# Optimization experiments

Measured on AMD Instinct MI355X. Metric: run time of the kernel, lower is better.

## Reference

```python
import jax, jax.numpy as jnp
import numpy as np
from jax import lax

N_NODES = 50000
N_EDGES = 800000
FEAT = 16
HID = 64
K = 32
N_CLASSES = 8


def _dconv(Xc, W, b, src, dst, norm_out, norm_in):
    """Dual-direction diffusion (Chebyshev-style) graph convolution.
    Xc: [N, Fin], W: [2, K, Fin, HID], norm_*: per-edge weights."""
    N = Xc.shape[0]

    def prop(x, s, d, ne):
        # out[i] = sum_{e: d[e]=i} ne[e] * x[s[e]]
        return jax.ops.segment_sum(x[s] * ne[:, None], d, num_segments=N)

    # k = 0 term (identity support, both directions)
    H = Xc @ (W[0, 0] + W[1, 0])
    # k = 1 term
    T1o = prop(Xc, src, dst, norm_out)   # forward diffusion
    T1i = prop(Xc, dst, src, norm_in)    # reverse diffusion
    H = H + T1o @ W[0, 1] + T1i @ W[1, 1]

    def step(carry, Wk):
        T0o, T1o, T0i, T1i, Hacc = carry
        T2o = 2.0 * prop(T1o, src, dst, norm_out) - T0o
        T2i = 2.0 * prop(T1i, dst, src, norm_in) - T0i
        Hacc = Hacc + T2o @ Wk[0] + T2i @ Wk[1]
        return (T1o, T2o, T1i, T2i, Hacc), None

    Wtail = jnp.stack([W[0, 2:], W[1, 2:]], axis=1)  # [K-2, 2, Fin, HID]
    (_, _, _, _, H), _ = lax.scan(step, (Xc, T1o, Xc, T1i, H), Wtail)
    return H + b


def setup_inputs() -> dict:
    key = jax.random.key(0)
    ks = jax.random.split(key, 8)
    Fin = FEAT + HID
    wscale = 1.0 / np.sqrt(Fin * K)
    x = jax.random.normal(ks[0], (N_NODES, FEAT), jnp.float32)
    edge_index = jax.random.randint(ks[1], (2, N_EDGES), 0, N_NODES, jnp.int64)
    W_z = jax.random.normal(ks[2], (2, K, Fin, HID), jnp.float32) * wscale
    W_r = jax.random.normal(ks[3], (2, K, Fin, HID), jnp.float32) * wscale
    W_h = jax.random.normal(ks[4], (2, K, Fin, HID), jnp.float32) * wscale
    lin_w = jax.random.normal(ks[5], (HID, N_CLASSES), jnp.float32) / np.sqrt(HID)
    return {
        "x": x, "edge_index": edge_index,
        "W_z": W_z, "b_z": jnp.zeros((HID,), jnp.float32),
        "W_r": W_r, "b_r": jnp.zeros((HID,), jnp.float32),
        "W_h": W_h, "b_h": jnp.zeros((HID,), jnp.float32),
        "lin_w": lin_w, "lin_b": jnp.zeros((N_CLASSES,), jnp.float32),
    }


def reference(x, edge_index, W_z, b_z, W_r, b_r, W_h, b_h, lin_w, lin_b):
    N = x.shape[0]
    src, dst = edge_index[0], edge_index[1]
    w = jnp.ones(src.shape[0], x.dtype)
    deg_out = jax.ops.segment_sum(w, src, num_segments=N)
    deg_in = jax.ops.segment_sum(w, dst, num_segments=N)
    inv = lambda d: jnp.where(d > 0, 1.0 / d, 0.0)
    norm_out = inv(deg_out)[src]  # per-edge 1/out-deg(source), forward walk
    norm_in = inv(deg_in)[dst]    # per-edge 1/in-deg(target), reverse walk

    # DCRNN GRU cell, single step, H initialized to zeros
    H0 = jnp.zeros((N, HID), x.dtype)
    Xc = jnp.concatenate([x, H0], axis=1)
    Z = jax.nn.sigmoid(_dconv(Xc, W_z, b_z, src, dst, norm_out, norm_in))
    R = jax.nn.sigmoid(_dconv(Xc, W_r, b_r, src, dst, norm_out, norm_in))
    Xh = jnp.concatenate([x, H0 * R], axis=1)
    Ht = jnp.tanh(_dconv(Xh, W_h, b_h, src, dst, norm_out, norm_in))
    H = Z * H0 + (1.0 - Z) * Ht

    return jax.nn.relu(H) @ lin_w + lin_b
```

## Files before the change

### kernel.cpp

```cpp
#include <hip/hip_runtime.h>
#include <math.h>

#define N_NODES 50000
#define N_EDGES 800000
#define FEAT    16
#define HID     64
#define KORD    32
#define NCLS    8

#define WSL     5120
#define SLOT    (N_NODES * FEAT)

typedef __attribute__((ext_vector_type(8))) short bf8_t;
typedef __attribute__((ext_vector_type(4))) float f32x4;

static constexpr size_t Aln(size_t x) { return (x + 255) & ~size_t(255); }

static constexpr size_t OFF_DEG_OUT = 0;
static constexpr size_t OFF_DEG_IN  = OFF_DEG_OUT + Aln(N_NODES * 4);
static constexpr size_t OFF_CUR_DST = OFF_DEG_IN  + Aln(N_NODES * 4);
static constexpr size_t OFF_CUR_SRC = OFF_CUR_DST + Aln(N_NODES * 4);
static constexpr size_t ZERO_BYTES  = OFF_CUR_SRC + Aln(N_NODES * 4);
static constexpr size_t OFF_OFF_DST = ZERO_BYTES;
static constexpr size_t OFF_OFF_SRC = OFF_OFF_DST + Aln((N_NODES + 1) * 4);
static constexpr size_t OFF_CSRD    = OFF_OFF_SRC + Aln((N_NODES + 1) * 4);
static constexpr size_t OFF_CSRS    = OFF_CSRD + Aln(N_EDGES * 4);
static constexpr size_t OFF_SLAB    = OFF_CSRS + Aln(N_EDGES * 4);
static constexpr size_t OFF_BSZH    = OFF_SLAB + Aln((size_t)64 * SLOT * 4);
static constexpr size_t OFF_BSZL    = OFF_BSZH + Aln((size_t)32 * 8 * 64 * 8 * 2);
static constexpr size_t WS_TOTAL    = OFF_BSZL + Aln((size_t)32 * 8 * 64 * 8 * 2);

__device__ __forceinline__ ushort f2bf(float v) {
    unsigned int b = __float_as_uint(v);
    b += 0x7FFFu + ((b >> 16) & 1u);
    return (ushort)(b >> 16);
}
__device__ __forceinline__ float bf2f(ushort h) {
    return __uint_as_float((unsigned int)h << 16);
}

__global__ void count_deg_kernel(const int* __restrict__ ei,
                                 int* __restrict__ deg_out, int* __restrict__ deg_in) {
    int e4 = blockIdx.x * blockDim.x + threadIdx.x;
    if (e4 * 4 >= N_EDGES) return;
    int4 s = *(const int4*)&ei[e4 * 4];
    int4 d = *(const int4*)&ei[N_EDGES + e4 * 4];
    atomicAdd(&deg_out[s.x], 1); atomicAdd(&deg_out[s.y], 1);
    atomicAdd(&deg_out[s.z], 1); atomicAdd(&deg_out[s.w], 1);
    atomicAdd(&deg_in[d.x], 1);  atomicAdd(&deg_in[d.y], 1);
    atomicAdd(&deg_in[d.z], 1);  atomicAdd(&deg_in[d.w], 1);
}

__global__ __launch_bounds__(1024) void scan_kernel(const int* __restrict__ degA, int* __restrict__ offA,
                                                    const int* __restrict__ degB, int* __restrict__ offB) {
    const int* deg = blockIdx.x ? degB : degA;
    int* off = blockIdx.x ? offB : offA;
    __shared__ int wsum[16];
    __shared__ int s_run;
    const int t = threadIdx.x, lane = t & 63, wid = t >> 6;
    if (t == 0) s_run = 0;
    __syncthreads();
    for (int base = 0; base < N_NODES; base += 1024) {
        int i = base + t;
        int v = (i < N_NODES) ? deg[i] : 0;
        int xv = v;
        #pragma unroll
        for (int d = 1; d < 64; d <<= 1) {
            int tt = __shfl_up(xv, d, 64);
            if (lane >= d) xv += tt;
        }
        if (lane == 63) wsum[wid] = xv;
        __syncthreads();
        int add = s_run;
        for (int w = 0; w < wid; ++w) add += wsum[w];
        if (i < N_NODES) off[i] = add + xv - v;
        __syncthreads();
        if (t == 1023) s_run = add + xv;
        __syncthreads();
    }
    if (t == 0) off[N_NODES] = s_run;
}

__global__ void fill_csr_kernel(const int* __restrict__ ei,
                                const int* __restrict__ deg_out, const int* __restrict__ deg_in,
                                const int* __restrict__ off_dst, const int* __restrict__ off_src,
                                int* __restrict__ cur_dst, int* __restrict__ cur_src,
                                unsigned int* __restrict__ csrd, unsigned int* __restrict__ csrs) {
    int e = blockIdx.x * blockDim.x + threadIdx.x;
    if (e >= N_EDGES) return;
    int s = ei[e], d = ei[N_EDGES + e];
    int p = off_dst[d] + atomicAdd(&cur_dst[d], 1);
    csrd[p] = ((unsigned int)deg_out[s] << 16) | (unsigned int)s;
    int q = off_src[s] + atomicAdd(&cur_src[s], 1);
    csrs[q] = ((unsigned int)deg_in[d] << 16) | (unsigned int)d;
}

__device__ __forceinline__ float4 gather4d(const unsigned int* __restrict__ csr, int beg, int end,
                                           int u, int fq, const float* __restrict__ src) {
    float4 acc = {0.f, 0.f, 0.f, 0.f};
    for (int e0 = beg; e0 < end; e0 += 16) {
        int ea = e0 + u, eb = e0 + 4 + u, ec = e0 + 8 + u, ed = e0 + 12 + u;
        unsigned int pa = (ea < end) ? csr[ea] : 0x10000u;
        unsigned int pb = (eb < end) ? csr[eb] : 0x10000u;
        unsigned int pc = (ec < end) ? csr[ec] : 0x10000u;
        unsigned int pd = (ed < end) ? csr[ed] : 0x10000u;
        float wa = (ea < end) ? 1.0f / (float)(pa >> 16) : 0.0f;
        float wb = (eb < end) ? 1.0f / (float)(pb >> 16) : 0.0f;
        float wc = (ec < end) ? 1.0f / (float)(pc >> 16) : 0.0f;
        float wd = (ed < end) ? 1.0f / (float)(pd >> 16) : 0.0f;
        const float4 ra = *(const float4*)&src[(pa & 0xFFFFu) * FEAT + fq * 4];
        const float4 rb = *(const float4*)&src[(pb & 0xFFFFu) * FEAT + fq * 4];
        const float4 rc = *(const float4*)&src[(pc & 0xFFFFu) * FEAT + fq * 4];
        const float4 rd = *(const float4*)&src[(pd & 0xFFFFu) * FEAT + fq * 4];
        acc.x += wa * ra.x + wb * rb.x + wc * rc.x + wd * rd.x;
        acc.y += wa * ra.y + wb * rb.y + wc * rc.y + wd * rd.y;
        acc.z += wa * ra.z + wb * rb.z + wc * rc.z + wd * rd.z;
        acc.w += wa * ra.w + wb * rb.w + wc * rc.w + wd * rd.w;
    }
    return acc;
}

__device__ __forceinline__ float4 reduce_u(float4 a) {
    a.x += __shfl_xor(a.x, 4); a.y += __shfl_xor(a.y, 4);
    a.z += __shfl_xor(a.z, 4); a.w += __shfl_xor(a.w, 4);
    a.x += __shfl_xor(a.x, 8); a.y += __shfl_xor(a.y, 8);
    a.z += __shfl_xor(a.z, 8); a.w += __shfl_xor(a.w, 8);
    return a;
}

__global__ __launch_bounds__(256) void init_kernel(
    const float* __restrict__ x,
    const int* __restrict__ off_dst, const unsigned int* __restrict__ csrd,
    const int* __restrict__ off_src, const unsigned int* __restrict__ csrs,
    float* __restrict__ slab) {
    const int dir = blockIdx.x & 1;
    const int bi  = blockIdx.x >> 1;
    const int* off = dir ? off_src : off_dst;
    const unsigned int* csr = dir ? csrs : csrd;
    const int t = threadIdx.x;
    const int g = t >> 4, l = t & 15, u = l >> 2, fq = l & 3;
    const int i = bi * 16 + g;
    const int b = off[i], e = off[i + 1];
    float4 a = reduce_u(gather4d(csr, b, e, u, fq, x));
    if (u == 0) {
        const int ro = i * FEAT + fq * 4;
        float4 xr = *(const float4*)&x[ro];
        *(float4*)&slab[(size_t)(dir * 32 + 0) * SLOT + ro] = xr;
        *(float4*)&slab[(size_t)(dir * 32 + 1) * SLOT + ro] = a;
    }
}

__global__ __launch_bounds__(256) void step_kernel(
    const int* __restrict__ off_dst, const unsigned int* __restrict__ csrd,
    const int* __restrict__ off_src, const unsigned int* __restrict__ csrs,
    float* __restrict__ slab, int k) {
    const int dir = blockIdx.x & 1;
    const int bi  = blockIdx.x >> 1;
    const int* off = dir ? off_src : off_dst;
    const unsigned int* csr = dir ? csrs : csrd;
    const float* prev = slab + (size_t)(dir * 32 + k - 1) * SLOT;
    const float* pp   = slab + (size_t)(dir * 32 + k - 2) * SLOT;
    float*       outp = slab + (size_t)(dir * 32 + k) * SLOT;
    const int t = threadIdx.x;
    const int g = t >> 4, l = t & 15, u = l >> 2, fq = l & 3;
    const int i = bi * 16 + g;
    const int b = off[i], e = off[i + 1];
    float4 a = reduce_u(gather4d(csr, b, e, u, fq, prev));
    if (u == 0) {
        const int ro = i * FEAT + fq * 4;
        float4 p = *(const float4*)&pp[ro];
        float4 t2;
        t2.x = 2.f * a.x - p.x; t2.y = 2.f * a.y - p.y;
        t2.z = 2.f * a.z - p.z; t2.w = 2.f * a.w - p.w;
        *(float4*)&outp[ro] = t2;
    }
}

__global__ void wswiz_kernel(const float* __restrict__ Wz, const float* __restrict__ Wh,
                             ushort* __restrict__ bszh, ushort* __restrict__ bszl) {
    int idx = blockIdx.x * blockDim.x + threadIdx.x;
    if (idx >= 32 * 8 * 64) return;
    int l  = idx & 63;
    int nc = (idx >> 6) & 7;
    int kc = idx >> 9;
    int si = kc * 2 + ((l >> 4) >> 1);
    int f0 = ((l >> 4) & 1) * 8;
    int c  = nc * 16 + (l & 15);
    const float* W = (c < 64) ? Wz : Wh;
    int cc = (c < 64) ? c : c - 64;
    ushort vh[8], vl[8];
    #pragma unroll
    for (int i = 0; i < 8; ++i) {
        float v = W[(size_t)si * WSL + (f0 + i) * 64 + cc];
        ushort h = f2bf(v);
        vh[i] = h;
        vl[i] = f2bf(v - bf2f(h));
    }
    ushort* dh = &bszh[(size_t)idx * 8];
    *(ushort4*)dh       = make_ushort4(vh[0], vh[1], vh[2], vh[3]);
    *(ushort4*)(dh + 4) = make_ushort4(vh[4], vh[5], vh[6], vh[7]);
    ushort* dl = &bszl[(size_t)idx * 8];
    *(ushort4*)dl       = make_ushort4(vl[0], vl[1], vl[2], vl[3]);
    *(ushort4*)(dl + 4) = make_ushort4(vl[4], vl[5], vl[6], vl[7]);
}

__device__ __forceinline__ void cvtA(const float* __restrict__ ap, bf8_t& aHi, bf8_t& aLo) {
    float4 a0 = *(const float4*)ap;
    float4 a1 = *(const float4*)(ap + 4);
    float av[8] = {a0.x, a0.y, a0.z, a0.w, a1.x, a1.y, a1.z, a1.w};
    #pragma unroll
    for (int i = 0; i < 8; ++i) {
        ushort h = f2bf(av[i]);
        aHi[i] = (short)h;
        aLo[i] = (short)f2bf(av[i] - bf2f(h));
    }
}

__global__ __launch_bounds__(512) void final_kernel(
    const float* __restrict__ slab, const ushort* __restrict__ bszh, const ushort* __restrict__ bszl,
    const float* __restrict__ bz, const float* __restrict__ bh,
    const float* __restrict__ lin_w, const float* __restrict__ lin_b,
    float* __restrict__ out) {
    __shared__ alignas(16) ushort sfrag[2][8192];
    const int t = threadIdx.x;
    const int w = t >> 6, l = t & 63;
    const int cl = l & 15, hi = l >> 4;
    const int n0 = blockIdx.x * 128 + w * 16;
    const int nodeA = n0 + cl;
    const bool ok = nodeA < N_NODES;
    const int siAdd = hi >> 1, f0 = (hi & 1) * 8;

    f32x4 acc[8];
    #pragma unroll
    for (int nc = 0; nc < 8; ++nc) {
        int c = nc * 16 + cl;
        float bias = (c < 64) ? bz[c] : bh[c - 64];
        acc[nc] = (f32x4){bias, bias, bias, bias};
    }

    {
        const uint4* sH = (const uint4*)(bszh);
        const uint4* sL = (const uint4*)(bszl);
        uint4* d = (uint4*)sfrag[0];
        d[t] = sH[t];
        d[t + 512] = sL[t];
    }
    __syncthreads();

    for (int kc = 0; kc < 32; ++kc) {
        const int buf = kc & 1;
        if (kc < 31) {
            const uint4* sH = (const uint4*)(bszh + (size_t)(kc + 1) * 4096);
            const uint4* sL = (const uint4*)(bszl + (size_t)(kc + 1) * 4096);
            uint4* d = (uint4*)sfrag[buf ^ 1];
            d[t] = sH[t];
            d[t + 512] = sL[t];
        }
        bf8_t aH = (bf8_t)0, aL = (bf8_t)0;
        if (ok) {
            int si = kc * 2 + siAdd;
            cvtA(&slab[(size_t)si * SLOT + nodeA * FEAT + f0], aH, aL);
        }
        const ushort* fb = sfrag[buf];
        #pragma unroll
        for (int nc = 0; nc < 8; ++nc) {
            bf8_t bHi = *(const bf8_t*)&fb[nc * 512 + l * 8];
            bf8_t bLo = *(const bf8_t*)&fb[4096 + nc * 512 + l * 8];
            acc[nc] = __builtin_amdgcn_mfma_f32_16x16x32_bf16(aH, bHi, acc[nc], 0, 0, 0);
            acc[nc] = __builtin_amdgcn_mfma_f32_16x16x32_bf16(aL, bHi, acc[nc], 0, 0, 0);
            acc[nc] = __builtin_amdgcn_mfma_f32_16x16x32_bf16(aH, bLo, acc[nc], 0, 0, 0);
        }
        __syncthreads();
    }

    float po[4][8];
    #pragma unroll
    for (int i = 0; i < 4; ++i)
        #pragma unroll
        for (int cls = 0; cls < 8; ++cls) po[i][cls] = 0.f;
    #pragma unroll
    for (int i = 0; i < 4; ++i) {
        #pragma unroll
        for (int nc = 0; nc < 4; ++nc) {
            float hz = acc[nc][i], hh = acc[nc + 4][i];
            float z  = 1.f / (1.f + __expf(-hz));
            float ht = tanhf(hh);
            float v  = fmaxf(0.f, (1.f - z) * ht);
            const float* lwr = &lin_w[(nc * 16 + cl) * 8];
            #pragma unroll
            for (int cls = 0; cls < 8; ++cls) po[i][cls] += v * lwr[cls];
        }
    }
    #pragma unroll
    for (int m = 1; m < 16; m <<= 1) {
        #pragma unroll
        for (int i = 0; i < 4; ++i)
            #pragma unroll
            for (int cls = 0; cls < 8; ++cls)
                po[i][cls] += __shfl_xor(po[i][cls], m, 16);
    }
    if (cl < 8) {
        #pragma unroll
        for (int i = 0; i < 4; ++i) {
            int node = n0 + hi * 4 + i;
            if (node < N_NODES) out[node * NCLS + cl] = po[i][cl] + lin_b[cl];
        }
    }
}

extern "C" void kernel_launch(void* const* d_in, const int* in_sizes, int n_in,
                              void* d_out, int out_size, void* d_ws, size_t ws_size,
                              hipStream_t stream) {
    const float* x   = (const float*)d_in[0];
    const int*   ei  = (const int*)d_in[1];
    const float* Wz  = (const float*)d_in[2];
    const float* bz  = (const float*)d_in[3];
    const float* Wh  = (const float*)d_in[6];
    const float* bh  = (const float*)d_in[7];
    const float* lw  = (const float*)d_in[8];
    const float* lb  = (const float*)d_in[9];
    float* out = (float*)d_out;
    char* ws = (char*)d_ws;

    int*  deg_out = (int*)(ws + OFF_DEG_OUT);
    int*  deg_in  = (int*)(ws + OFF_DEG_IN);
    int*  cur_dst = (int*)(ws + OFF_CUR_DST);
    int*  cur_src = (int*)(ws + OFF_CUR_SRC);
    int*  off_dst = (int*)(ws + OFF_OFF_DST);
    int*  off_src = (int*)(ws + OFF_OFF_SRC);
    unsigned int* csrd = (unsigned int*)(ws + OFF_CSRD);
    unsigned int* csrs = (unsigned int*)(ws + OFF_CSRS);
    float*  slab = (float*)(ws + OFF_SLAB);
    ushort* bszh = (ushort*)(ws + OFF_BSZH);
    ushort* bszl = (ushort*)(ws + OFF_BSZL);

    hipMemsetAsync(ws, 0, ZERO_BYTES, stream);

    const int EB = (N_EDGES + 255) / 256;
    const int NB16 = N_NODES / 16;
    count_deg_kernel<<<(N_EDGES / 4 + 255) / 256, 256, 0, stream>>>(ei, deg_out, deg_in);
    scan_kernel<<<2, 1024, 0, stream>>>(deg_in, off_dst, deg_out, off_src);
    fill_csr_kernel<<<EB, 256, 0, stream>>>(ei, deg_out, deg_in, off_dst, off_src,
                                            cur_dst, cur_src, csrd, csrs);
    wswiz_kernel<<<(32 * 8 * 64 + 255) / 256, 256, 0, stream>>>(Wz, Wh, bszh, bszl);
    init_kernel<<<NB16 * 2, 256, 0, stream>>>(x, off_dst, csrd, off_src, csrs, slab);

    for (int k = 2; k < KORD; ++k)
        step_kernel<<<NB16 * 2, 256, 0, stream>>>(off_dst, csrd, off_src, csrs, slab, k);

    final_kernel<<<(N_NODES + 127) / 128, 512, 0, stream>>>(slab, bszh, bszl,
                                                            bz, bh, lw, lb, out);
}
```

Before: 781.3 us.

## Pad CSR rows to multiples of four and privatize degree counting

Each CSR row is padded to a multiple of four entries, so the gather loop can fetch four packed neighbor entries with a single 16-byte load instead of four scalar loads. Row ends now come from the degree arrays rather than the next offset. Degree counting is split across eight private copies that a new reduce kernel then sums, which spreads out atomic contention. This costs more workspace memory, one extra kernel launch and the memset of the larger private buffers.

After: 797.2 us. 1.02x slower.

```diff
diff --git a/kernel.cpp b/kernel.cpp
--- a/kernel.cpp
+++ b/kernel.cpp
@@ -10,22 +10,25 @@
 
 #define WSL     5120
 #define SLOT    (N_NODES * FEAT)
+#define CSR_CAP (N_EDGES + 4 * N_NODES + 16)
 
 typedef __attribute__((ext_vector_type(8))) short bf8_t;
 typedef __attribute__((ext_vector_type(4))) float f32x4;
 
 static constexpr size_t Aln(size_t x) { return (x + 255) & ~size_t(255); }
 
-static constexpr size_t OFF_DEG_OUT = 0;
-static constexpr size_t OFF_DEG_IN  = OFF_DEG_OUT + Aln(N_NODES * 4);
-static constexpr size_t OFF_CUR_DST = OFF_DEG_IN  + Aln(N_NODES * 4);
+static constexpr size_t OFF_DEGPO   = 0;
+static constexpr size_t OFF_DEGPI   = OFF_DEGPO + Aln((size_t)8 * N_NODES * 4);
+static constexpr size_t OFF_CUR_DST = OFF_DEGPI + Aln((size_t)8 * N_NODES * 4);
 static constexpr size_t OFF_CUR_SRC = OFF_CUR_DST + Aln(N_NODES * 4);
 static constexpr size_t ZERO_BYTES  = OFF_CUR_SRC + Aln(N_NODES * 4);
-static constexpr size_t OFF_OFF_DST = ZERO_BYTES;
+static constexpr size_t OFF_DEG_OUT = ZERO_BYTES;
+static constexpr size_t OFF_DEG_IN  = OFF_DEG_OUT + Aln(N_NODES * 4);
+static constexpr size_t OFF_OFF_DST = OFF_DEG_IN + Aln((N_NODES + 1) * 4);
 static constexpr size_t OFF_OFF_SRC = OFF_OFF_DST + Aln((N_NODES + 1) * 4);
 static constexpr size_t OFF_CSRD    = OFF_OFF_SRC + Aln((N_NODES + 1) * 4);
-static constexpr size_t OFF_CSRS    = OFF_CSRD + Aln(N_EDGES * 4);
-static constexpr size_t OFF_SLAB    = OFF_CSRS + Aln(N_EDGES * 4);
+static constexpr size_t OFF_CSRS    = OFF_CSRD + Aln((size_t)CSR_CAP * 4);
+static constexpr size_t OFF_SLAB    = OFF_CSRS + Aln((size_t)CSR_CAP * 4);
 static constexpr size_t OFF_BSZH    = OFF_SLAB + Aln((size_t)64 * SLOT * 4);
 static constexpr size_t OFF_BSZL    = OFF_BSZH + Aln((size_t)32 * 8 * 64 * 8 * 2);
 static constexpr size_t WS_TOTAL    = OFF_BSZL + Aln((size_t)32 * 8 * 64 * 8 * 2);
@@ -40,15 +43,30 @@
 }
 
 __global__ void count_deg_kernel(const int* __restrict__ ei,
-                                 int* __restrict__ deg_out, int* __restrict__ deg_in) {
+                                 int* __restrict__ privO, int* __restrict__ privI) {
     int e4 = blockIdx.x * blockDim.x + threadIdx.x;
     if (e4 * 4 >= N_EDGES) return;
+    const int c = (blockIdx.x & 7) * N_NODES;
     int4 s = *(const int4*)&ei[e4 * 4];
     int4 d = *(const int4*)&ei[N_EDGES + e4 * 4];
-    atomicAdd(&deg_out[s.x], 1); atomicAdd(&deg_out[s.y], 1);
-    atomicAdd(&deg_out[s.z], 1); atomicAdd(&deg_out[s.w], 1);
-    atomicAdd(&deg_in[d.x], 1);  atomicAdd(&deg_in[d.y], 1);
-    atomicAdd(&deg_in[d.z], 1);  atomicAdd(&deg_in[d.w], 1);
+    atomicAdd(&privO[c + s.x], 1); atomicAdd(&privO[c + s.y], 1);
+    atomicAdd(&privO[c + s.z], 1); atomicAdd(&privO[c + s.w], 1);
+    atomicAdd(&privI[c + d.x], 1); atomicAdd(&privI[c + d.y], 1);
+    atomicAdd(&privI[c + d.z], 1); atomicAdd(&privI[c + d.w], 1);
+}
+
+__global__ void reduce_deg_kernel(const int* __restrict__ privO, const int* __restrict__ privI,
+                                  int* __restrict__ deg_out, int* __restrict__ deg_in) {
+    int i = blockIdx.x * blockDim.x + threadIdx.x;
+    if (i >= N_NODES) return;
+    int so = 0, si = 0;
+    #pragma unroll
+    for (int c = 0; c < 8; ++c) {
+        so += privO[c * N_NODES + i];
+        si += privI[c * N_NODES + i];
+    }
+    deg_out[i] = so;
+    deg_in[i] = si;
 }
 
 __global__ __launch_bounds__(1024) void scan_kernel(const int* __restrict__ degA, int* __restrict__ offA,
@@ -62,7 +80,7 @@
     __syncthreads();
     for (int base = 0; base < N_NODES; base += 1024) {
         int i = base + t;
-        int v = (i < N_NODES) ? deg[i] : 0;
+        int v = (i < N_NODES) ? ((deg[i] + 3) & ~3) : 0;
         int xv = v;
         #pragma unroll
         for (int d = 1; d < 64; d <<= 1) {
@@ -95,27 +113,28 @@
     csrs[q] = ((unsigned int)deg_in[d] << 16) | (unsigned int)d;
 }
 
-__device__ __forceinline__ float4 gather4d(const unsigned int* __restrict__ csr, int beg, int end,
+__device__ __forceinline__ float4 gather4v(const unsigned int* __restrict__ csr, int beg, int end,
                                            int u, int fq, const float* __restrict__ src) {
     float4 acc = {0.f, 0.f, 0.f, 0.f};
     for (int e0 = beg; e0 < end; e0 += 16) {
-        int ea = e0 + u, eb = e0 + 4 + u, ec = e0 + 8 + u, ed = e0 + 12 + u;
-        unsigned int pa = (ea < end) ? csr[ea] : 0x10000u;
-        unsigned int pb = (eb < end) ? csr[eb] : 0x10000u;
-        unsigned int pc = (ec < end) ? csr[ec] : 0x10000u;
-        unsigned int pd = (ed < end) ? csr[ed] : 0x10000u;
-        float wa = (ea < end) ? 1.0f / (float)(pa >> 16) : 0.0f;
-        float wb = (eb < end) ? 1.0f / (float)(pb >> 16) : 0.0f;
-        float wc = (ec < end) ? 1.0f / (float)(pc >> 16) : 0.0f;
-        float wd = (ed < end) ? 1.0f / (float)(pd >> 16) : 0.0f;
-        const float4 ra = *(const float4*)&src[(pa & 0xFFFFu) * FEAT + fq * 4];
-        const float4 rb = *(const float4*)&src[(pb & 0xFFFFu) * FEAT + fq * 4];
-        const float4 rc = *(const float4*)&src[(pc & 0xFFFFu) * FEAT + fq * 4];
-        const float4 rd = *(const float4*)&src[(pd & 0xFFFFu) * FEAT + fq * 4];
-        acc.x += wa * ra.x + wb * rb.x + wc * rc.x + wd * rd.x;
-        acc.y += wa * ra.y + wb * rb.y + wc * rc.y + wd * rd.y;
-        acc.z += wa * ra.z + wb * rb.z + wc * rc.z + wd * rd.z;
-        acc.w += wa * ra.w + wb * rb.w + wc * rc.w + wd * rd.w;
+        const int eb = e0 + 4 * u;
+        uint4 q = *(const uint4*)&csr[eb];
+        unsigned int pk0 = (eb < end)     ? q.x : 0x10000u;
+        unsigned int pk1 = (eb + 1 < end) ? q.y : 0x10000u;
+        unsigned int pk2 = (eb + 2 < end) ? q.z : 0x10000u;
+        unsigned int pk3 = (eb + 3 < end) ? q.w : 0x10000u;
+        float w0 = (eb < end)     ? 1.0f / (float)(pk0 >> 16) : 0.0f;
+        float w1 = (eb + 1 < end) ? 1.0f / (float)(pk1 >> 16) : 0.0f;
+        float w2 = (eb + 2 < end) ? 1.0f / (float)(pk2 >> 16) : 0.0f;
+        float w3 = (eb + 3 < end) ? 1.0f / (float)(pk3 >> 16) : 0.0f;
+        const float4 r0 = *(const float4*)&src[(pk0 & 0xFFFFu) * FEAT + fq * 4];
+        const float4 r1 = *(const float4*)&src[(pk1 & 0xFFFFu) * FEAT + fq * 4];
+        const float4 r2 = *(const float4*)&src[(pk2 & 0xFFFFu) * FEAT + fq * 4];
+        const float4 r3 = *(const float4*)&src[(pk3 & 0xFFFFu) * FEAT + fq * 4];
+        acc.x += w0 * r0.x + w1 * r1.x + w2 * r2.x + w3 * r3.x;
+        acc.y += w0 * r0.y + w1 * r1.y + w2 * r2.y + w3 * r3.y;
+        acc.z += w0 * r0.z + w1 * r1.z + w2 * r2.z + w3 * r3.z;
+        acc.w += w0 * r0.w + w1 * r1.w + w2 * r2.w + w3 * r3.w;
     }
     return acc;
 }
@@ -132,16 +151,18 @@
     const float* __restrict__ x,
     const int* __restrict__ off_dst, const unsigned int* __restrict__ csrd,
     const int* __restrict__ off_src, const unsigned int* __restrict__ csrs,
+    const int* __restrict__ deg_out, const int* __restrict__ deg_in,
     float* __restrict__ slab) {
     const int dir = blockIdx.x & 1;
     const int bi  = blockIdx.x >> 1;
     const int* off = dir ? off_src : off_dst;
     const unsigned int* csr = dir ? csrs : csrd;
+    const int* dga = dir ? deg_out : deg_in;
     const int t = threadIdx.x;
     const int g = t >> 4, l = t & 15, u = l >> 2, fq = l & 3;
     const int i = bi * 16 + g;
-    const int b = off[i], e = off[i + 1];
-    float4 a = reduce_u(gather4d(csr, b, e, u, fq, x));
+    const int b = off[i], e = b + dga[i];
+    float4 a = reduce_u(gather4v(csr, b, e, u, fq, x));
     if (u == 0) {
         const int ro = i * FEAT + fq * 4;
         float4 xr = *(const float4*)&x[ro];
@@ -153,19 +174,21 @@
 __global__ __launch_bounds__(256) void step_kernel(
     const int* __restrict__ off_dst, const unsigned int* __restrict__ csrd,
     const int* __restrict__ off_src, const unsigned int* __restrict__ csrs,
+    const int* __restrict__ deg_out, const int* __restrict__ deg_in,
     float* __restrict__ slab, int k) {
     const int dir = blockIdx.x & 1;
     const int bi  = blockIdx.x >> 1;
     const int* off = dir ? off_src : off_dst;
     const unsigned int* csr = dir ? csrs : csrd;
+    const int* dga = dir ? deg_out : deg_in;
     const float* prev = slab + (size_t)(dir * 32 + k - 1) * SLOT;
     const float* pp   = slab + (size_t)(dir * 32 + k - 2) * SLOT;
     float*       outp = slab + (size_t)(dir * 32 + k) * SLOT;
     const int t = threadIdx.x;
     const int g = t >> 4, l = t & 15, u = l >> 2, fq = l & 3;
     const int i = bi * 16 + g;
-    const int b = off[i], e = off[i + 1];
-    float4 a = reduce_u(gather4d(csr, b, e, u, fq, prev));
+    const int b = off[i], e = b + dga[i];
+    float4 a = reduce_u(gather4v(csr, b, e, u, fq, prev));
     if (u == 0) {
         const int ro = i * FEAT + fq * 4;
         float4 p = *(const float4*)&pp[ro];
@@ -322,10 +345,12 @@
     float* out = (float*)d_out;
     char* ws = (char*)d_ws;
 
+    int*  privO   = (int*)(ws + OFF_DEGPO);
+    int*  privI   = (int*)(ws + OFF_DEGPI);
+    int*  cur_dst = (int*)(ws + OFF_CUR_DST);
+    int*  cur_src = (int*)(ws + OFF_CUR_SRC);
     int*  deg_out = (int*)(ws + OFF_DEG_OUT);
     int*  deg_in  = (int*)(ws + OFF_DEG_IN);
-    int*  cur_dst = (int*)(ws + OFF_CUR_DST);
-    int*  cur_src = (int*)(ws + OFF_CUR_SRC);
     int*  off_dst = (int*)(ws + OFF_OFF_DST);
     int*  off_src = (int*)(ws + OFF_OFF_SRC);
     unsigned int* csrd = (unsigned int*)(ws + OFF_CSRD);
@@ -338,15 +363,18 @@
 
     const int EB = (N_EDGES + 255) / 256;
     const int NB16 = N_NODES / 16;
-    count_deg_kernel<<<(N_EDGES / 4 + 255) / 256, 256, 0, stream>>>(ei, deg_out, deg_in);
+    count_deg_kernel<<<(N_EDGES / 4 + 255) / 256, 256, 0, stream>>>(ei, privO, privI);
+    reduce_deg_kernel<<<(N_NODES + 255) / 256, 256, 0, stream>>>(privO, privI, deg_out, deg_in);
     scan_kernel<<<2, 1024, 0, stream>>>(deg_in, off_dst, deg_out, off_src);
     fill_csr_kernel<<<EB, 256, 0, stream>>>(ei, deg_out, deg_in, off_dst, off_src,
                                             cur_dst, cur_src, csrd, csrs);
     wswiz_kernel<<<(32 * 8 * 64 + 255) / 256, 256, 0, stream>>>(Wz, Wh, bszh, bszl);
-    init_kernel<<<NB16 * 2, 256, 0, stream>>>(x, off_dst, csrd, off_src, csrs, slab);
+    init_kernel<<<NB16 * 2, 256, 0, stream>>>(x, off_dst, csrd, off_src, csrs,
+                                              deg_out, deg_in, slab);
 
     for (int k = 2; k < KORD; ++k)
-        step_kernel<<<NB16 * 2, 256, 0, stream>>>(off_dst, csrd, off_src, csrs, slab, k);
+        step_kernel<<<NB16 * 2, 256, 0, stream>>>(off_dst, csrd, off_src, csrs,
+                                                  deg_out, deg_in, slab, k);
 
     final_kernel<<<(N_NODES + 127) / 128, 512, 0, stream>>>(slab, bszh, bszl,
                                                             bz, bh, lw, lb, out);
```
